# Kernel optimization log

Hardware: AMD Instinct MI355X
Metric: run time of the kernel (lower is better)

Reference implementation:

```python
import jax, jax.numpy as jnp
import numpy as np

EMB = 256
HEADS = 8
HEAD_DIM = EMB // HEADS


def setup_inputs() -> dict:
    key = jax.random.key(0)
    k1, k2, k3, k4, k5 = jax.random.split(key, 5)
    stdv = 1.0 / np.sqrt(HEAD_DIM)  # uniform(-stdv, stdv) init as in torch module
    stdv_o = 1.0 / np.sqrt(EMB)
    return {
        "query": jax.random.normal(k1, (2, 4096, EMB), dtype=jnp.float32),
        "query_weight": jax.random.uniform(k2, (HEADS, EMB, HEAD_DIM), jnp.float32, -stdv, stdv),
        "key_weight": jax.random.uniform(k3, (HEADS, EMB, HEAD_DIM), jnp.float32, -stdv, stdv),
        "value_weight": jax.random.uniform(k4, (HEADS, EMB, HEAD_DIM), jnp.float32, -stdv, stdv),
        "output_weight": jax.random.uniform(k5, (HEADS, HEAD_DIM, EMB), jnp.float32, -stdv_o, stdv_o),
    }


def reference(query, query_weight, key_weight, value_weight, output_weight):
    # self-attention: key = value = query
    norm = 1.0 / np.sqrt(HEAD_DIM)
    # per-head projections: [h, b, s, d_head]
    Q = jnp.einsum("bsd,hde->hbse", query, query_weight)
    K = jnp.einsum("bsd,hde->hbse", query, key_weight)
    V = jnp.einsum("bsd,hde->hbse", query, value_weight)
    # scores [h, b, q, k] -- explicitly materialized as in the original
    U = norm * jnp.einsum("hbqe,hbke->hbqk", Q, K)
    attention = jax.nn.softmax(U, axis=-1)
    heads = jnp.einsum("hbqk,hbke->hbqe", attention, V)
    # output projection: concat heads then mm with output_weight.reshape(h*e, EMB)
    out = jnp.einsum("hbqe,heo->bqo", heads, output_weight)
    return (out, attention)
```

## Files before the change

### kernel.cpp

```cpp
#include <hip/hip_runtime.h>
#include <math.h>

#define EMB 256
#define HEADS 8
#define HD 32
#define BATCH 2
#define SEQ 4096
#define QSCALE 0.25504672075827703f

typedef __attribute__((ext_vector_type(8))) _Float16 f16x8;
typedef __attribute__((ext_vector_type(4))) _Float16 f16x4;
typedef __attribute__((ext_vector_type(2))) __fp16 fp16x2_native;
typedef __attribute__((ext_vector_type(4))) float f32x4;
typedef unsigned int uint_t;

__device__ __forceinline__ uint_t pk16(float a, float b) {
    union { fp16x2_native h; uint_t u; } cv;
    cv.h = __builtin_amdgcn_cvt_pkrtz(a, b);
    return cv.u;
}

#define MFMA16(A, B, C) __builtin_amdgcn_mfma_f32_16x16x32_f16(A, B, C, 0, 0, 0)
#define MFMA16K16(A, B, C) __builtin_amdgcn_mfma_f32_16x16x16f16(A, B, C, 0, 0, 0)

__global__ __launch_bounds__(256) void prep_x_kernel(
    const float* __restrict__ q, _Float16* __restrict__ Xh, _Float16* __restrict__ Xl)
{
    const int i = (blockIdx.x * 256 + threadIdx.x) * 8;
    float4 v0 = *(const float4*)(q + i);
    float4 v1 = *(const float4*)(q + i + 4);
    float xs[8] = {v0.x, v0.y, v0.z, v0.w, v1.x, v1.y, v1.z, v1.w};
    f16x8 hv, lv;
    #pragma unroll
    for (int j = 0; j < 8; j++) {
        _Float16 h = (_Float16)xs[j];
        hv[j] = h;
        lv[j] = (_Float16)(xs[j] - (float)h);
    }
    *(f16x8*)(Xh + i) = hv;
    *(f16x8*)(Xl + i) = lv;
}

__global__ __launch_bounds__(256) void prep_w_kernel(
    const float* __restrict__ wq, const float* __restrict__ wk,
    const float* __restrict__ wv, const float* __restrict__ wo,
    _Float16* __restrict__ Wth, _Float16* __restrict__ Wtl,
    _Float16* __restrict__ WoTh, _Float16* __restrict__ WoTl)
{
    for (int t = blockIdx.x * 256 + threadIdx.x; t < 262144; t += 256 * 256) {
        if (t < 196608) {
            int d = t & 255, e = (t >> 8) & 31, ph = t >> 13;
            int p = ph >> 3, h = ph & 7;
            const float* w = (p == 0) ? wq : (p == 1 ? wk : wv);
            float val = w[h * 8192 + d * 32 + e] * ((p == 0) ? QSCALE : 1.0f);
            _Float16 hi = (_Float16)val;
            Wth[t] = hi;
            Wtl[t] = (_Float16)(val - (float)hi);
        } else {
            int t2 = t - 196608;
            int he = t2 & 255, o = t2 >> 8;
            float val = wo[(he >> 5) * 8192 + (he & 31) * 256 + o];
            _Float16 hi = (_Float16)val;
            WoTh[t2] = hi;
            WoTl[t2] = (_Float16)(val - (float)hi);
        }
    }
}

__global__ __launch_bounds__(256) void qkv_gemm_kernel(
    const _Float16* __restrict__ Xh, const _Float16* __restrict__ Xl,
    const _Float16* __restrict__ Wth, const _Float16* __restrict__ Wtl,
    _Float16* __restrict__ Qf, _Float16* __restrict__ Kf, _Float16* __restrict__ VT)
{
    __shared__ _Float16 st[4][16][32];
    const int t = threadIdx.x, w = t >> 6, l = t & 63, lo4 = l & 15, g = l >> 4;
    const int tile = blockIdx.x, ph = blockIdx.y, p = ph >> 3, h = ph & 7;
    const int r0 = tile * 64 + w * 16;
    const int b = (tile * 64) >> 12;
    const int s_base = (tile * 64) & (SEQ - 1);
    const int hb = h * BATCH + b;

    f16x8 Ah[8], Al[8];
    const size_t xoff = (size_t)(r0 + lo4) * 256 + g * 8;
    #pragma unroll
    for (int kc = 0; kc < 8; kc++) {
        Ah[kc] = *(const f16x8*)(Xh + xoff + kc * 32);
        Al[kc] = *(const f16x8*)(Xl + xoff + kc * 32);
    }

    f32x4 D[2];
    #pragma unroll
    for (int ct = 0; ct < 2; ct++) {
        f32x4 acc = {0.f, 0.f, 0.f, 0.f};
        const size_t woff = (size_t)(ph * 32 + ct * 16 + lo4) * 256 + g * 8;
        #pragma unroll
        for (int kc = 0; kc < 8; kc++) {
            f16x8 Bh = *(const f16x8*)(Wth + woff + kc * 32);
            f16x8 Bl = *(const f16x8*)(Wtl + woff + kc * 32);
            acc = MFMA16(Ah[kc], Bh, acc);
            acc = MFMA16(Al[kc], Bh, acc);
            acc = MFMA16(Ah[kc], Bl, acc);
        }
        D[ct] = acc;
    }

    if (p < 2) {
        #pragma unroll
        for (int ct = 0; ct < 2; ct++)
            #pragma unroll
            for (int r = 0; r < 4; r++)
                st[w][g * 4 + r][ct * 16 + lo4] = (_Float16)D[ct][r];
        __syncthreads();
        _Float16* dst = (p == 0) ? Qf : Kf;
        const int rl = t >> 2, e8 = (t & 3) * 8;
        *(f16x8*)(dst + ((size_t)hb * SEQ + s_base + rl) * HD + e8) =
            *(f16x8*)&st[rl >> 4][rl & 15][e8];
    } else {
        #pragma unroll
        for (int ct = 0; ct < 2; ct++) {
            f16x4 v;
            #pragma unroll
            for (int r = 0; r < 4; r++) v[r] = (_Float16)D[ct][r];
            *(f16x4*)(VT + ((size_t)hb * HD + ct * 16 + lo4) * SEQ + s_base + w * 16 + g * 4) = v;
        }
    }
}

__global__ __launch_bounds__(256) void attn_kernel(
    const _Float16* __restrict__ Qf, const _Float16* __restrict__ Kf,
    const _Float16* __restrict__ VT,
    float* __restrict__ attn_out,
    _Float16* __restrict__ heads)
{
    __shared__ float lred[4][2][16];
    __shared__ float Hred[4][32][33];

    const int tid = threadIdx.x;
    const int w = tid >> 6;
    const int l = tid & 63;
    const int lo4 = l & 15;
    const int g = l >> 4;
    const int bid = blockIdx.x;
    const int xcd = bid & 7;
    const int j = bid >> 3;
    const int hb = xcd + 8 * (j >> 7);
    const int q0 = (j & 127) * 32;

    const _Float16* Qb = Qf + (size_t)hb * SEQ * HD;
    const _Float16* Kb = Kf + (size_t)hb * SEQ * HD;
    const _Float16* Vb = VT + (size_t)hb * HD * SEQ;

    const f16x8 Bq0 = *(const f16x8*)(Qb + (size_t)(q0 + lo4) * HD + g * 8);
    const f16x8 Bq1 = *(const f16x8*)(Qb + (size_t)(q0 + 16 + lo4) * HD + g * 8);

    const int c_lo = w * 32, c_hi = c_lo + 32;

    float ls0 = 0.f, ls1 = 0.f;
    for (int c = c_lo; c < c_hi; c++) {
        const int k0 = c * 32;
        #pragma unroll
        for (int s = 0; s < 2; s++) {
            f16x8 Ak = *(const f16x8*)(Kb + (size_t)(k0 + s * 16 + lo4) * HD + g * 8);
            f32x4 D0 = {0.f, 0.f, 0.f, 0.f}, D1 = {0.f, 0.f, 0.f, 0.f};
            D0 = MFMA16(Ak, Bq0, D0);
            D1 = MFMA16(Ak, Bq1, D1);
            ls0 += exp2f(D0[0]) + exp2f(D0[1]) + exp2f(D0[2]) + exp2f(D0[3]);
            ls1 += exp2f(D1[0]) + exp2f(D1[1]) + exp2f(D1[2]) + exp2f(D1[3]);
        }
    }
    ls0 += __shfl_xor(ls0, 16, 64); ls0 += __shfl_xor(ls0, 32, 64);
    ls1 += __shfl_xor(ls1, 16, 64); ls1 += __shfl_xor(ls1, 32, 64);
    if (l < 16) { lred[w][0][lo4] = ls0; lred[w][1][lo4] = ls1; }
    __syncthreads();
    const float inv0 = 1.0f / (lred[0][0][lo4] + lred[1][0][lo4] + lred[2][0][lo4] + lred[3][0][lo4]);
    const float inv1 = 1.0f / (lred[0][1][lo4] + lred[1][1][lo4] + lred[2][1][lo4] + lred[3][1][lo4]);

    f32x4 H00 = {0.f,0.f,0.f,0.f}, H01 = {0.f,0.f,0.f,0.f};
    f32x4 H10 = {0.f,0.f,0.f,0.f}, H11 = {0.f,0.f,0.f,0.f};
    float* ar0 = attn_out + ((size_t)hb * SEQ + q0 + lo4) * SEQ;
    float* ar1 = ar0 + (size_t)16 * SEQ;

    for (int c = c_lo; c < c_hi; c++) {
        const int k0 = c * 32;
        #pragma unroll
        for (int s = 0; s < 2; s++) {
            f16x8 Ak = *(const f16x8*)(Kb + (size_t)(k0 + s * 16 + lo4) * HD + g * 8);
            f32x4 D0 = {0.f, 0.f, 0.f, 0.f}, D1 = {0.f, 0.f, 0.f, 0.f};
            D0 = MFMA16(Ak, Bq0, D0);
            D1 = MFMA16(Ak, Bq1, D1);
            float p00 = exp2f(D0[0]) * inv0, p01 = exp2f(D0[1]) * inv0;
            float p02 = exp2f(D0[2]) * inv0, p03 = exp2f(D0[3]) * inv0;
            float p10 = exp2f(D1[0]) * inv1, p11 = exp2f(D1[1]) * inv1;
            float p12 = exp2f(D1[2]) * inv1, p13 = exp2f(D1[3]) * inv1;
            *(float4*)(ar0 + k0 + s * 16 + g * 4) = make_float4(p00, p01, p02, p03);
            *(float4*)(ar1 + k0 + s * 16 + g * 4) = make_float4(p10, p11, p12, p13);
            union { f16x4 v; uint_t u[2]; } P0, P1;
            P0.u[0] = pk16(p00, p01); P0.u[1] = pk16(p02, p03);
            P1.u[0] = pk16(p10, p11); P1.u[1] = pk16(p12, p13);
            f16x4 Av0 = *(const f16x4*)(Vb + (size_t)lo4 * SEQ + k0 + s * 16 + g * 4);
            f16x4 Av1 = *(const f16x4*)(Vb + (size_t)(16 + lo4) * SEQ + k0 + s * 16 + g * 4);
            H00 = MFMA16K16(Av0, P0.v, H00);
            H01 = MFMA16K16(Av1, P0.v, H01);
            H10 = MFMA16K16(Av0, P1.v, H10);
            H11 = MFMA16K16(Av1, P1.v, H11);
        }
    }

    #pragma unroll
    for (int r = 0; r < 4; r++) {
        Hred[w][lo4][g * 4 + r]            = H00[r];
        Hred[w][lo4][16 + g * 4 + r]       = H01[r];
        Hred[w][16 + lo4][g * 4 + r]       = H10[r];
        Hred[w][16 + lo4][16 + g * 4 + r]  = H11[r];
    }
    __syncthreads();
    for (int i = tid; i < 32 * 32; i += 256) {
        int qq = i >> 5, e = i & 31;
        float sum = Hred[0][qq][e] + Hred[1][qq][e] + Hred[2][qq][e] + Hred[3][qq][e];
        heads[((size_t)hb * SEQ + q0 + qq) * HD + e] = (_Float16)sum;
    }
}

__global__ __launch_bounds__(256) void out_gemm_kernel(
    const _Float16* __restrict__ Hf,
    const _Float16* __restrict__ WoTh, const _Float16* __restrict__ WoTl,
    float* __restrict__ out)
{
    const int t = threadIdx.x, w = t >> 6, l = t & 63, lo4 = l & 15, g = l >> 4;
    const int r0 = blockIdx.x * 64 + w * 16;
    const int b = r0 >> 12;
    const int sb = r0 & (SEQ - 1);

    f16x8 A[8];
    #pragma unroll
    for (int kc = 0; kc < 8; kc++)
        A[kc] = *(const f16x8*)(Hf + (((size_t)(kc * BATCH + b)) * SEQ + sb + lo4) * HD + g * 8);

    for (int ct = 0; ct < 16; ct++) {
        f32x4 acc = {0.f, 0.f, 0.f, 0.f};
        const size_t woff = (size_t)(ct * 16 + lo4) * 256 + g * 8;
        #pragma unroll
        for (int kc = 0; kc < 8; kc++) {
            acc = MFMA16(A[kc], *(const f16x8*)(WoTh + woff + kc * 32), acc);
            acc = MFMA16(A[kc], *(const f16x8*)(WoTl + woff + kc * 32), acc);
        }
        #pragma unroll
        for (int r = 0; r < 4; r++)
            out[(size_t)(r0 + g * 4 + r) * 256 + ct * 16 + lo4] = acc[r];
    }
}

extern "C" void kernel_launch(void* const* d_in, const int* in_sizes, int n_in,
                              void* d_out, int out_size, void* d_ws, size_t ws_size,
                              hipStream_t stream) {
    const float* query = (const float*)d_in[0];
    const float* wq = (const float*)d_in[1];
    const float* wk = (const float*)d_in[2];
    const float* wv = (const float*)d_in[3];
    const float* wo = (const float*)d_in[4];
    float* out = (float*)d_out;
    float* attn_out = out + (size_t)BATCH * SEQ * EMB;

    _Float16* ws = (_Float16*)d_ws;
    const size_t nx  = (size_t)BATCH * SEQ * EMB;
    const size_t per = (size_t)HEADS * BATCH * SEQ * HD;
    _Float16* Xh   = ws;
    _Float16* Xl   = Xh + nx;
    _Float16* Wth  = Xl + nx;
    _Float16* Wtl  = Wth + 196608;
    _Float16* WoTh = Wtl + 196608;
    _Float16* WoTl = WoTh + 65536;
    _Float16* Qf   = WoTl + 65536;
    _Float16* Kf   = Qf + per;
    _Float16* VT   = Kf + per;
    _Float16* Hf   = VT + per;

    prep_x_kernel<<<(int)(nx / (256 * 8)), 256, 0, stream>>>(query, Xh, Xl);
    prep_w_kernel<<<256, 256, 0, stream>>>(wq, wk, wv, wo, Wth, Wtl, WoTh, WoTl);
    qkv_gemm_kernel<<<dim3((BATCH * SEQ) / 64, 3 * HEADS), 256, 0, stream>>>(
        Xh, Xl, Wth, Wtl, Qf, Kf, VT);
    attn_kernel<<<HEADS * BATCH * (SEQ / 32), 256, 0, stream>>>(
        Qf, Kf, VT, attn_out, Hf);
    out_gemm_kernel<<<(BATCH * SEQ) / 64, 256, 0, stream>>>(Hf, WoTh, WoTl, out);
}
```

Baseline: 436.5 us.

## Give each wave its own 16 query rows over full key range, drop LDS reductions

The attention kernel now assigns each wave 16 distinct query rows and sweeps all 4096 keys, instead of splitting keys across waves for 32 shared rows. This removes the shared-memory row-sum and head-output reductions and both __syncthreads, and uses 64-query blocks with half as many blocks. The PV product switches from 16x16x16 to 16x16x32 MFMA, with probabilities rearranged across lanes via shuffles. In exchange, K/V reuse across the two query halves per wave is lost and each wave runs a longer serial loop with shuffle overhead.

Measured after the change: 566.5 us. 1.3x slower.

```diff
diff --git a/kernel.cpp b/kernel.cpp
--- a/kernel.cpp
+++ b/kernel.cpp
@@ -21,7 +21,6 @@
 }
 
 #define MFMA16(A, B, C) __builtin_amdgcn_mfma_f32_16x16x32_f16(A, B, C, 0, 0, 0)
-#define MFMA16K16(A, B, C) __builtin_amdgcn_mfma_f32_16x16x16f16(A, B, C, 0, 0, 0)
 
 __global__ __launch_bounds__(256) void prep_x_kernel(
     const float* __restrict__ q, _Float16* __restrict__ Xh, _Float16* __restrict__ Xl)
@@ -132,9 +131,6 @@
     float* __restrict__ attn_out,
     _Float16* __restrict__ heads)
 {
-    __shared__ float lred[4][2][16];
-    __shared__ float Hred[4][32][33];
-
     const int tid = threadIdx.x;
     const int w = tid >> 6;
     const int l = tid & 63;
@@ -143,82 +139,69 @@
     const int bid = blockIdx.x;
     const int xcd = bid & 7;
     const int j = bid >> 3;
-    const int hb = xcd + 8 * (j >> 7);
-    const int q0 = (j & 127) * 32;
+    const int hb = xcd + 8 * (j >> 6);
+    const int q0 = (j & 63) * 64;
+    const int qw = q0 + w * 16;
 
     const _Float16* Qb = Qf + (size_t)hb * SEQ * HD;
     const _Float16* Kb = Kf + (size_t)hb * SEQ * HD;
     const _Float16* Vb = VT + (size_t)hb * HD * SEQ;
 
-    const f16x8 Bq0 = *(const f16x8*)(Qb + (size_t)(q0 + lo4) * HD + g * 8);
-    const f16x8 Bq1 = *(const f16x8*)(Qb + (size_t)(q0 + 16 + lo4) * HD + g * 8);
-
-    const int c_lo = w * 32, c_hi = c_lo + 32;
-
-    float ls0 = 0.f, ls1 = 0.f;
-    for (int c = c_lo; c < c_hi; c++) {
+    const f16x8 Bq = *(const f16x8*)(Qb + (size_t)(qw + lo4) * HD + g * 8);
+
+    float ls = 0.f;
+    for (int c = 0; c < 128; c++) {
         const int k0 = c * 32;
         #pragma unroll
         for (int s = 0; s < 2; s++) {
             f16x8 Ak = *(const f16x8*)(Kb + (size_t)(k0 + s * 16 + lo4) * HD + g * 8);
-            f32x4 D0 = {0.f, 0.f, 0.f, 0.f}, D1 = {0.f, 0.f, 0.f, 0.f};
-            D0 = MFMA16(Ak, Bq0, D0);
-            D1 = MFMA16(Ak, Bq1, D1);
-            ls0 += exp2f(D0[0]) + exp2f(D0[1]) + exp2f(D0[2]) + exp2f(D0[3]);
-            ls1 += exp2f(D1[0]) + exp2f(D1[1]) + exp2f(D1[2]) + exp2f(D1[3]);
-        }
-    }
-    ls0 += __shfl_xor(ls0, 16, 64); ls0 += __shfl_xor(ls0, 32, 64);
-    ls1 += __shfl_xor(ls1, 16, 64); ls1 += __shfl_xor(ls1, 32, 64);
-    if (l < 16) { lred[w][0][lo4] = ls0; lred[w][1][lo4] = ls1; }
-    __syncthreads();
-    const float inv0 = 1.0f / (lred[0][0][lo4] + lred[1][0][lo4] + lred[2][0][lo4] + lred[3][0][lo4]);
-    const float inv1 = 1.0f / (lred[0][1][lo4] + lred[1][1][lo4] + lred[2][1][lo4] + lred[3][1][lo4]);
-
-    f32x4 H00 = {0.f,0.f,0.f,0.f}, H01 = {0.f,0.f,0.f,0.f};
-    f32x4 H10 = {0.f,0.f,0.f,0.f}, H11 = {0.f,0.f,0.f,0.f};
-    float* ar0 = attn_out + ((size_t)hb * SEQ + q0 + lo4) * SEQ;
-    float* ar1 = ar0 + (size_t)16 * SEQ;
-
-    for (int c = c_lo; c < c_hi; c++) {
+            f32x4 D = {0.f, 0.f, 0.f, 0.f};
+            D = MFMA16(Ak, Bq, D);
+            ls += exp2f(D[0]) + exp2f(D[1]) + exp2f(D[2]) + exp2f(D[3]);
+        }
+    }
+    ls += __shfl_xor(ls, 16, 64);
+    ls += __shfl_xor(ls, 32, 64);
+    const float inv = 1.0f / ls;
+
+    f32x4 H0 = {0.f,0.f,0.f,0.f}, H1 = {0.f,0.f,0.f,0.f};
+    float* ar = attn_out + ((size_t)hb * SEQ + qw + lo4) * SEQ;
+    const int src0 = lo4 + ((g & 1) * 2) * 16;
+    const int src1 = src0 + 16;
+
+    for (int c = 0; c < 128; c++) {
         const int k0 = c * 32;
+        uint_t w0[2], w1[2];
         #pragma unroll
         for (int s = 0; s < 2; s++) {
             f16x8 Ak = *(const f16x8*)(Kb + (size_t)(k0 + s * 16 + lo4) * HD + g * 8);
-            f32x4 D0 = {0.f, 0.f, 0.f, 0.f}, D1 = {0.f, 0.f, 0.f, 0.f};
-            D0 = MFMA16(Ak, Bq0, D0);
-            D1 = MFMA16(Ak, Bq1, D1);
-            float p00 = exp2f(D0[0]) * inv0, p01 = exp2f(D0[1]) * inv0;
-            float p02 = exp2f(D0[2]) * inv0, p03 = exp2f(D0[3]) * inv0;
-            float p10 = exp2f(D1[0]) * inv1, p11 = exp2f(D1[1]) * inv1;
-            float p12 = exp2f(D1[2]) * inv1, p13 = exp2f(D1[3]) * inv1;
-            *(float4*)(ar0 + k0 + s * 16 + g * 4) = make_float4(p00, p01, p02, p03);
-            *(float4*)(ar1 + k0 + s * 16 + g * 4) = make_float4(p10, p11, p12, p13);
-            union { f16x4 v; uint_t u[2]; } P0, P1;
-            P0.u[0] = pk16(p00, p01); P0.u[1] = pk16(p02, p03);
-            P1.u[0] = pk16(p10, p11); P1.u[1] = pk16(p12, p13);
-            f16x4 Av0 = *(const f16x4*)(Vb + (size_t)lo4 * SEQ + k0 + s * 16 + g * 4);
-            f16x4 Av1 = *(const f16x4*)(Vb + (size_t)(16 + lo4) * SEQ + k0 + s * 16 + g * 4);
-            H00 = MFMA16K16(Av0, P0.v, H00);
-            H01 = MFMA16K16(Av1, P0.v, H01);
-            H10 = MFMA16K16(Av0, P1.v, H10);
-            H11 = MFMA16K16(Av1, P1.v, H11);
-        }
-    }
-
-    #pragma unroll
-    for (int r = 0; r < 4; r++) {
-        Hred[w][lo4][g * 4 + r]            = H00[r];
-        Hred[w][lo4][16 + g * 4 + r]       = H01[r];
-        Hred[w][16 + lo4][g * 4 + r]       = H10[r];
-        Hred[w][16 + lo4][16 + g * 4 + r]  = H11[r];
-    }
-    __syncthreads();
-    for (int i = tid; i < 32 * 32; i += 256) {
-        int qq = i >> 5, e = i & 31;
-        float sum = Hred[0][qq][e] + Hred[1][qq][e] + Hred[2][qq][e] + Hred[3][qq][e];
-        heads[((size_t)hb * SEQ + q0 + qq) * HD + e] = (_Float16)sum;
-    }
+            f32x4 D = {0.f, 0.f, 0.f, 0.f};
+            D = MFMA16(Ak, Bq, D);
+            float p0 = exp2f(D[0]) * inv, p1 = exp2f(D[1]) * inv;
+            float p2 = exp2f(D[2]) * inv, p3 = exp2f(D[3]) * inv;
+            *(float4*)(ar + k0 + s * 16 + g * 4) = make_float4(p0, p1, p2, p3);
+            w0[s] = pk16(p0, p1); w1[s] = pk16(p2, p3);
+        }
+        union { f16x8 v; uint_t u[4]; } P;
+        {
+            uint_t a, b2;
+            a = __shfl(w0[0], src0, 64); b2 = __shfl(w0[1], src0, 64); P.u[0] = (g >= 2) ? b2 : a;
+            a = __shfl(w1[0], src0, 64); b2 = __shfl(w1[1], src0, 64); P.u[1] = (g >= 2) ? b2 : a;
+            a = __shfl(w0[0], src1, 64); b2 = __shfl(w0[1], src1, 64); P.u[2] = (g >= 2) ? b2 : a;
+            a = __shfl(w1[0], src1, 64); b2 = __shfl(w1[1], src1, 64); P.u[3] = (g >= 2) ? b2 : a;
+        }
+        f16x8 Av0 = *(const f16x8*)(Vb + (size_t)lo4 * SEQ + k0 + g * 8);
+        f16x8 Av1 = *(const f16x8*)(Vb + (size_t)(16 + lo4) * SEQ + k0 + g * 8);
+        H0 = MFMA16(Av0, P.v, H0);
+        H1 = MFMA16(Av1, P.v, H1);
+    }
+
+    _Float16* hrow = heads + ((size_t)hb * SEQ + qw + lo4) * HD;
+    f16x4 h0, h1;
+    #pragma unroll
+    for (int r = 0; r < 4; r++) { h0[r] = (_Float16)H0[r]; h1[r] = (_Float16)H1[r]; }
+    *(f16x4*)(hrow + g * 4) = h0;
+    *(f16x4*)(hrow + 16 + g * 4) = h1;
 }
 
 __global__ __launch_bounds__(256) void out_gemm_kernel(
@@ -279,7 +262,7 @@
     prep_w_kernel<<<256, 256, 0, stream>>>(wq, wk, wv, wo, Wth, Wtl, WoTh, WoTl);
     qkv_gemm_kernel<<<dim3((BATCH * SEQ) / 64, 3 * HEADS), 256, 0, stream>>>(
         Xh, Xl, Wth, Wtl, Qf, Kf, VT);
-    attn_kernel<<<HEADS * BATCH * (SEQ / 32), 256, 0, stream>>>(
+    attn_kernel<<<HEADS * BATCH * (SEQ / 64), 256, 0, stream>>>(
         Qf, Kf, VT, attn_out, Hf);
     out_gemm_kernel<<<(BATCH * SEQ) / 64, 256, 0, stream>>>(Hf, WoTh, WoTl, out);
 }
```
